# Kernel tuning notes

Measured on AMD Instinct MI355X. Metric: run time of the kernel, lower is better.

Reference implementation:

```python
import jax, jax.numpy as jnp
import numpy as np

HIDDEN = 2048
T = 8192
WASHOUT = 200
SPECTRAL_RADIUS = 0.9


def setup_inputs() -> dict:
    key = jax.random.key(0)
    k_u, k_in, k_res, k_out = jax.random.split(key, 4)
    u = jax.random.normal(k_u, (T,), dtype=jnp.float32)
    # w_in ~ Uniform(-0.5, 0.5) * input_scaling (1.0)
    w_in = jax.random.uniform(k_in, (HIDDEN,), dtype=jnp.float32) - 0.5
    # w_res ~ Uniform(-0.5, 0.5), rescaled to spectral radius 0.9 (init-time buffer construction)
    w_res = np.asarray(jax.random.uniform(k_res, (HIDDEN, HIDDEN), dtype=jnp.float32)) - 0.5
    sr = float(np.max(np.abs(np.linalg.eigvals(w_res.astype(np.float64)))))
    w_res = jnp.asarray((w_res * (SPECTRAL_RADIUS / sr)).astype(np.float32))
    # trained readout stand-in (module stores it as buffer w_out, used by pinv predict path)
    w_out = jax.random.normal(k_out, (HIDDEN,), dtype=jnp.float32) * 0.05
    return {"u": u, "w_in": w_in, "w_res": w_res, "w_out": w_out}


def reference(u, w_in, w_res, w_out):
    # x_{t} = tanh(w_in * u_t + w_res @ x_{t-1}), x_{-1} = 0
    def step(x, u_t):
        x = jnp.tanh(w_in * u_t + w_res @ x)
        return x, x

    x0 = jnp.zeros((HIDDEN,), dtype=w_res.dtype)
    _, X = jax.lax.scan(step, x0, u)  # X: [T, HIDDEN]
    # pinv predict path: X[washout:] @ w_out
    return X[WASHOUT:] @ w_out
```

## Files before the change

### kernel.cpp

```cpp
#include <hip/hip_runtime.h>

#define HIDDEN   2048
#define T_STEPS  8192
#define WASHOUT  200
#define NWG      64
#define NTHR     1024
#define NWAVE    (NTHR / 64)
#define ROWS_PER_WG   (HIDDEN / NWG)
#define ROWS_PER_WAVE (ROWS_PER_WG / NWAVE)
#define NCHUNK   16
#define NREPL    8
#define REPL     (2 * HIDDEN)


#define DPP_ADD(x, ctrl) ((x) + __int_as_float(__builtin_amdgcn_update_dpp( \
    0, __float_as_int(x), ctrl, 0xF, 0xF, true)))

typedef unsigned uint4v __attribute__((ext_vector_type(4)));
typedef unsigned uint2v __attribute__((ext_vector_type(2)));

#define PERMLANE_SUM_1632(h)                                         \
  {                                                                  \
    uint2v s16 = __builtin_amdgcn_permlane16_swap(                   \
        __float_as_uint(h), __float_as_uint(h), false, false);       \
    h = __uint_as_float(s16.x) + __uint_as_float(s16.y);             \
    uint2v s32 = __builtin_amdgcn_permlane32_swap(                   \
        __float_as_uint(h), __float_as_uint(h), false, false);       \
    h = __uint_as_float(s32.x) + __uint_as_float(s32.y);             \
  }

__global__ __launch_bounds__(NTHR, 1) void esn_main(
    const float* __restrict__ u,
    const float* __restrict__ w_in,
    const float* __restrict__ w_res,
    const float* __restrict__ w_out,
    float* __restrict__ out,
    unsigned long long* __restrict__ pairs,
    int nrepl)
{
  const int g  = blockIdx.x;
  const int j  = threadIdx.x;
  const int wv = j >> 6;
  const int l  = j & 63;

  unsigned xcc;
  asm("s_getreg_b32 %0, hwreg(HW_REG_XCC_ID)" : "=s"(xcc));
  const unsigned ri = xcc & (unsigned)(nrepl - 1);
  unsigned long long* __restrict__ myrep = pairs + (size_t)ri * REPL;

  __shared__ float x_s[2][HIDDEN];
  __shared__ float u_s[T_STEPS];
  __shared__ float fresh[ROWS_PER_WG];

#pragma unroll
  for (int k = 0; k < T_STEPS / NTHR; ++k) u_s[j + NTHR * k] = u[j + NTHR * k];

  const int r0 = g * ROWS_PER_WG + wv * ROWS_PER_WAVE;

  float wreg[ROWS_PER_WAVE][2 * NCHUNK];
#pragma unroll
  for (int i = 0; i < ROWS_PER_WAVE; ++i) {
#pragma unroll
    for (int c = 0; c < NCHUNK; ++c) {
      const float2 a = *(const float2*)&w_res[(r0 + i) * HIDDEN + c * 128 + 2 * l];
      wreg[i][2 * c + 0] = a.x; wreg[i][2 * c + 1] = a.y;
    }
  }
#pragma unroll
  for (int i = 0; i < ROWS_PER_WAVE; ++i)
#pragma unroll
    for (int k = 0; k < 2 * NCHUNK; ++k)
      asm volatile("" : "+v"(wreg[i][k]));

  const float winl = w_in[r0 + (l & 1)];
  const float wol  = (wv == 8 && l < 32) ? w_out[g * 32 + l] : 0.f;

  __syncthreads();

  for (int t = 0; t < T_STEPS; ++t) {
    float d0 = 0.f, d1 = 0.f;
    const unsigned b = (unsigned)((t - 1) & 1);
    if (t > 0) {
      const unsigned want = (unsigned)(t - 1);
      const unsigned long long* bp = myrep + b * HIDDEN + (wv << 7) + 2 * l;
      uint4v A;
      for (;;) {
        asm volatile(
            "global_load_dwordx4 %0, %1, off sc1\n\t"
            "s_waitcnt vmcnt(0)"
            : "=&v"(A)
            : "v"(bp)
            : "memory");
        if ((A.x == want) & (A.z == want)) break;
      }
      float2 xv;
      xv.x = __uint_as_float(A.y);
      xv.y = __uint_as_float(A.w);
      *(float2*)&x_s[b][(wv << 7) + 2 * l] = xv;
    }
    __syncthreads();

    if (t > 0) {
#pragma unroll
      for (int c = 0; c < NCHUNK; ++c) {
        const float2 x2 = *(const float2*)&x_s[b][(c << 7) + 2 * l];
        d0 = fmaf(wreg[0][2 * c + 0], x2.x, d0);
        d0 = fmaf(wreg[0][2 * c + 1], x2.y, d0);
        d1 = fmaf(wreg[1][2 * c + 0], x2.x, d1);
        d1 = fmaf(wreg[1][2 * c + 1], x2.y, d1);
      }
    }

    float e0 = DPP_ADD(d0, 0xB1);
    float e1 = DPP_ADD(d1, 0xB1);
    float h = (l & 1) ? e1 : e0;
    h = DPP_ADD(h, 0x4E);
    h = DPP_ADD(h, 0x124);
    h = DPP_ADD(h, 0x128);
    PERMLANE_SUM_1632(h)

    const float ut = u_s[t];
    if (l < ROWS_PER_WAVE) {
      const float a = fmaf(winl, ut, h);
      float z;
      asm("v_exp_f32 %0, %1" : "=v"(z) : "v"(a * 2.885390082f));
      float r;
      asm("v_rcp_f32 %0, %1" : "=v"(r) : "v"(z + 1.0f));
      fresh[wv * ROWS_PER_WAVE + l] = fmaf(-2.0f, r, 1.0f);
    }
    __syncthreads();

    if (wv < nrepl && l < ROWS_PER_WG) {
      const unsigned long long pk =
          ((unsigned long long)__float_as_uint(fresh[l]) << 32) | (unsigned)t;
      __hip_atomic_store(
          pairs + (size_t)wv * REPL + (t & 1) * HIDDEN + g * ROWS_PER_WG + l,
          pk, __ATOMIC_RELAXED, __HIP_MEMORY_SCOPE_AGENT);
    }
    if (wv == 8 && t >= WASHOUT) {
      float part = (l < 32) ? fresh[l] * wol : 0.f;
      part = DPP_ADD(part, 0xB1);
      part = DPP_ADD(part, 0x4E);
      part = DPP_ADD(part, 0x124);
      part = DPP_ADD(part, 0x128);
      PERMLANE_SUM_1632(part)
      if (l == 0) atomicAdd(&out[t - WASHOUT], part);
    }
  }
}

extern "C" void kernel_launch(void* const* d_in, const int* in_sizes, int n_in,
                              void* d_out, int out_size, void* d_ws, size_t ws_size,
                              hipStream_t stream) {
  const float* u     = (const float*)d_in[0];
  const float* w_in  = (const float*)d_in[1];
  const float* w_res = (const float*)d_in[2];
  const float* w_out = (const float*)d_in[3];
  float* out = (float*)d_out;
  unsigned long long* pairs = (unsigned long long*)d_ws;

  const int nrepl =
      (ws_size >= (size_t)NREPL * REPL * sizeof(unsigned long long)) ? NREPL : 1;

  hipMemsetAsync(out, 0, (size_t)out_size * sizeof(float), stream);
  esn_main<<<NWG, NTHR, 0, stream>>>(u, w_in, w_res, w_out, out, pairs, nrepl);
}
```

Measured before the change: 14.47 ms.

## Have each wave poll the full state vector directly, dropping the LDS exchange

```diff
diff --git a/kernel.cpp b/kernel.cpp
--- a/kernel.cpp
+++ b/kernel.cpp
@@ -4,11 +4,11 @@
 #define T_STEPS  8192
 #define WASHOUT  200
 #define NWG      64
-#define NTHR     1024
+#define NTHR     512
 #define NWAVE    (NTHR / 64)
 #define ROWS_PER_WG   (HIDDEN / NWG)
 #define ROWS_PER_WAVE (ROWS_PER_WG / NWAVE)
-#define NCHUNK   16
+#define NSUB     4
 #define NREPL    8
 #define REPL     (2 * HIDDEN)
 
@@ -27,6 +27,58 @@
     uint2v s32 = __builtin_amdgcn_permlane32_swap(                   \
         __float_as_uint(h), __float_as_uint(h), false, false);       \
     h = __uint_as_float(s32.x) + __uint_as_float(s32.y);             \
+  }
+
+#define POLLSUB(s)                                                        \
+  {                                                                       \
+    const unsigned long long* bp = base + (s) * 512;                      \
+    uint4v A0, A1, A2, A3;                  \
+    for (;;) {                                                            \
+      asm volatile(                                                       \
+          "global_load_dwordx4 %0, %4, off sc1\n\t"                       \
+          "global_load_dwordx4 %1, %4, off offset:1024 sc1\n\t"           \
+          "global_load_dwordx4 %2, %4, off offset:2048 sc1\n\t"           \
+          "global_load_dwordx4 %3, %4, off offset:3072 sc1\n\t"           \
+          "s_waitcnt vmcnt(0)"                                            \
+          : "=&v"(A0), "=&v"(A1), "=&v"(A2), "=&v"(A3)                    \
+          : "v"(bp) : "memory");                                          \
+      if (((A0.x == want) & (A0.z == want) &                              \
+           (A1.x == want) & (A1.z == want)) &                             \
+          ((A2.x == want) & (A2.z == want) &                              \
+           (A3.x == want) & (A3.z == want))) break;                       \
+    }                                                                     \
+    d0 = fmaf(wreg[0][8*(s)+0], __uint_as_float(A0.y), d0);               \
+    d0 = fmaf(wreg[0][8*(s)+1], __uint_as_float(A0.w), d0);               \
+    d0 = fmaf(wreg[0][8*(s)+2], __uint_as_float(A1.y), d0);               \
+    d0 = fmaf(wreg[0][8*(s)+3], __uint_as_float(A1.w), d0);               \
+    d0 = fmaf(wreg[0][8*(s)+4], __uint_as_float(A2.y), d0);               \
+    d0 = fmaf(wreg[0][8*(s)+5], __uint_as_float(A2.w), d0);               \
+    d0 = fmaf(wreg[0][8*(s)+6], __uint_as_float(A3.y), d0);               \
+    d0 = fmaf(wreg[0][8*(s)+7], __uint_as_float(A3.w), d0);               \
+    d1 = fmaf(wreg[1][8*(s)+0], __uint_as_float(A0.y), d1);               \
+    d1 = fmaf(wreg[1][8*(s)+1], __uint_as_float(A0.w), d1);               \
+    d1 = fmaf(wreg[1][8*(s)+2], __uint_as_float(A1.y), d1);               \
+    d1 = fmaf(wreg[1][8*(s)+3], __uint_as_float(A1.w), d1);               \
+    d1 = fmaf(wreg[1][8*(s)+4], __uint_as_float(A2.y), d1);               \
+    d1 = fmaf(wreg[1][8*(s)+5], __uint_as_float(A2.w), d1);               \
+    d1 = fmaf(wreg[1][8*(s)+6], __uint_as_float(A3.y), d1);               \
+    d1 = fmaf(wreg[1][8*(s)+7], __uint_as_float(A3.w), d1);               \
+    d2 = fmaf(wreg[2][8*(s)+0], __uint_as_float(A0.y), d2);               \
+    d2 = fmaf(wreg[2][8*(s)+1], __uint_as_float(A0.w), d2);               \
+    d2 = fmaf(wreg[2][8*(s)+2], __uint_as_float(A1.y), d2);               \
+    d2 = fmaf(wreg[2][8*(s)+3], __uint_as_float(A1.w), d2);               \
+    d2 = fmaf(wreg[2][8*(s)+4], __uint_as_float(A2.y), d2);               \
+    d2 = fmaf(wreg[2][8*(s)+5], __uint_as_float(A2.w), d2);               \
+    d2 = fmaf(wreg[2][8*(s)+6], __uint_as_float(A3.y), d2);               \
+    d2 = fmaf(wreg[2][8*(s)+7], __uint_as_float(A3.w), d2);               \
+    d3 = fmaf(wreg[3][8*(s)+0], __uint_as_float(A0.y), d3);               \
+    d3 = fmaf(wreg[3][8*(s)+1], __uint_as_float(A0.w), d3);               \
+    d3 = fmaf(wreg[3][8*(s)+2], __uint_as_float(A1.y), d3);               \
+    d3 = fmaf(wreg[3][8*(s)+3], __uint_as_float(A1.w), d3);               \
+    d3 = fmaf(wreg[3][8*(s)+4], __uint_as_float(A2.y), d3);               \
+    d3 = fmaf(wreg[3][8*(s)+5], __uint_as_float(A2.w), d3);               \
+    d3 = fmaf(wreg[3][8*(s)+6], __uint_as_float(A3.y), d3);               \
+    d3 = fmaf(wreg[3][8*(s)+7], __uint_as_float(A3.w), d3);               \
   }
 
 __global__ __launch_bounds__(NTHR, 1) void esn_main(
@@ -48,7 +100,6 @@
   const unsigned ri = xcc & (unsigned)(nrepl - 1);
   unsigned long long* __restrict__ myrep = pairs + (size_t)ri * REPL;
 
-  __shared__ float x_s[2][HIDDEN];
   __shared__ float u_s[T_STEPS];
   __shared__ float fresh[ROWS_PER_WG];
 
@@ -57,64 +108,52 @@
 
   const int r0 = g * ROWS_PER_WG + wv * ROWS_PER_WAVE;
 
-  float wreg[ROWS_PER_WAVE][2 * NCHUNK];
+  float wreg[ROWS_PER_WAVE][8 * NSUB];
 #pragma unroll
   for (int i = 0; i < ROWS_PER_WAVE; ++i) {
 #pragma unroll
-    for (int c = 0; c < NCHUNK; ++c) {
-      const float2 a = *(const float2*)&w_res[(r0 + i) * HIDDEN + c * 128 + 2 * l];
-      wreg[i][2 * c + 0] = a.x; wreg[i][2 * c + 1] = a.y;
+    for (int s = 0; s < NSUB; ++s) {
+#pragma unroll
+      for (int k = 0; k < 4; ++k) {
+        const float2 a =
+            *(const float2*)&w_res[(r0 + i) * HIDDEN + s * 512 + k * 128 + 2 * l];
+        wreg[i][8 * s + 2 * k + 0] = a.x;
+        wreg[i][8 * s + 2 * k + 1] = a.y;
+      }
     }
   }
 #pragma unroll
   for (int i = 0; i < ROWS_PER_WAVE; ++i)
 #pragma unroll
-    for (int k = 0; k < 2 * NCHUNK; ++k)
+    for (int k = 0; k < 8 * NSUB; ++k)
       asm volatile("" : "+v"(wreg[i][k]));
 
-  const float winl = w_in[r0 + (l & 1)];
-  const float wol  = (wv == 8 && l < 32) ? w_out[g * 32 + l] : 0.f;
+  const float winl = w_in[r0 + (l & 3)];
+  const float wol  = (wv == 1 && l < 32) ? w_out[g * 32 + l] : 0.f;
 
   __syncthreads();
 
   for (int t = 0; t < T_STEPS; ++t) {
-    float d0 = 0.f, d1 = 0.f;
-    const unsigned b = (unsigned)((t - 1) & 1);
+    float d0 = 0.f, d1 = 0.f, d2 = 0.f, d3 = 0.f;
     if (t > 0) {
       const unsigned want = (unsigned)(t - 1);
-      const unsigned long long* bp = myrep + b * HIDDEN + (wv << 7) + 2 * l;
-      uint4v A;
-      for (;;) {
-        asm volatile(
-            "global_load_dwordx4 %0, %1, off sc1\n\t"
-            "s_waitcnt vmcnt(0)"
-            : "=&v"(A)
-            : "v"(bp)
-            : "memory");
-        if ((A.x == want) & (A.z == want)) break;
-      }
-      float2 xv;
-      xv.x = __uint_as_float(A.y);
-      xv.y = __uint_as_float(A.w);
-      *(float2*)&x_s[b][(wv << 7) + 2 * l] = xv;
-    }
-    __syncthreads();
-
-    if (t > 0) {
-#pragma unroll
-      for (int c = 0; c < NCHUNK; ++c) {
-        const float2 x2 = *(const float2*)&x_s[b][(c << 7) + 2 * l];
-        d0 = fmaf(wreg[0][2 * c + 0], x2.x, d0);
-        d0 = fmaf(wreg[0][2 * c + 1], x2.y, d0);
-        d1 = fmaf(wreg[1][2 * c + 0], x2.x, d1);
-        d1 = fmaf(wreg[1][2 * c + 1], x2.y, d1);
-      }
+      const unsigned long long* base =
+          myrep + (unsigned)((t - 1) & 1) * HIDDEN + 2 * l;
+      POLLSUB(0)
+      POLLSUB(1)
+      POLLSUB(2)
+      POLLSUB(3)
     }
 
     float e0 = DPP_ADD(d0, 0xB1);
     float e1 = DPP_ADD(d1, 0xB1);
-    float h = (l & 1) ? e1 : e0;
-    h = DPP_ADD(h, 0x4E);
+    float e2 = DPP_ADD(d2, 0xB1);
+    float e3 = DPP_ADD(d3, 0xB1);
+    float f0 = (l & 1) ? e1 : e0;
+    float f1 = (l & 1) ? e3 : e2;
+    f0 = DPP_ADD(f0, 0x4E);
+    f1 = DPP_ADD(f1, 0x4E);
+    float h = (l & 2) ? f1 : f0;
     h = DPP_ADD(h, 0x124);
     h = DPP_ADD(h, 0x128);
     PERMLANE_SUM_1632(h)
@@ -137,7 +176,7 @@
           pairs + (size_t)wv * REPL + (t & 1) * HIDDEN + g * ROWS_PER_WG + l,
           pk, __ATOMIC_RELAXED, __HIP_MEMORY_SCOPE_AGENT);
     }
-    if (wv == 8 && t >= WASHOUT) {
+    if (wv == 1 && t >= WASHOUT) {
       float part = (l < 32) ? fresh[l] * wol : 0.f;
       part = DPP_ADD(part, 0xB1);
       part = DPP_ADD(part, 0x4E);
```

After: 20.51 ms. 41.7% more time.
